# Performance work log

Hardware: AMD Instinct MI355X
Metric: run time of the kernel (lower is better)

## Reference

```python
import jax, jax.numpy as jnp
import numpy as np

D_MODEL = 1024
N_HEADS = 16
D_K = D_MODEL // N_HEADS


def setup_inputs() -> dict:
    key = jax.random.key(0)
    ks = jax.random.split(key, 12)
    B, S = 2, 2048
    scale = 1.0 / np.sqrt(D_MODEL)
    inp = {
        "q": jax.random.normal(ks[0], (B, S, D_MODEL), jnp.float32),
        "k": jax.random.normal(ks[1], (B, S, D_MODEL), jnp.float32),
        "v": jax.random.normal(ks[2], (B, S, D_MODEL), jnp.float32),
        "k_pe": jax.random.normal(ks[3], (N_HEADS, D_K, S), jnp.float32),
        "Wq": jax.random.normal(ks[4], (D_MODEL, D_MODEL), jnp.float32) * scale,
        "bq": jnp.zeros((D_MODEL,), jnp.float32),
        "Wk": jax.random.normal(ks[5], (D_MODEL, D_MODEL), jnp.float32) * scale,
        "bk": jnp.zeros((D_MODEL,), jnp.float32),
        "Wv": jax.random.normal(ks[6], (D_MODEL, D_MODEL), jnp.float32) * scale,
        "bv": jnp.zeros((D_MODEL,), jnp.float32),
        "Wo": jax.random.normal(ks[7], (D_MODEL, D_MODEL), jnp.float32) * scale,
        "bo": jnp.zeros((D_MODEL,), jnp.float32),
    }
    return inp


def reference(q, k, v, k_pe, Wq, bq, Wk, bk, Wv, bv, Wo, bo):
    B, S, _ = q.shape
    # projections -> [B, H, S, d_k]
    def split_heads(x):
        return x.reshape(B, S, N_HEADS, D_K).transpose(0, 2, 1, 3)
    qh = split_heads(q @ Wq + bq)
    kh = split_heads(k @ Wk + bk)
    vh = split_heads(v @ Wv + bv)
    # content scores + relative positional scores (two matmuls, summed)
    scores = jnp.einsum("bhsd,bhtd->bhst", qh, kh)
    scores = scores + jnp.einsum("bhsd,hdt->bhst", qh, k_pe)
    scores = scores / jnp.sqrt(jnp.asarray(D_K, qh.dtype))
    attn = jax.nn.softmax(scores, axis=-1)
    out = jnp.einsum("bhst,bhtd->bhsd", attn, vh)  # [B,H,S,d_k]
    out = out.transpose(0, 2, 1, 3).reshape(B, S, D_MODEL)
    return out @ Wo + bo
```

## Files before the change

### kernel.cpp

```cpp
#include <hip/hip_runtime.h>
#include <stdint.h>
#include <math.h>

typedef __bf16 bf16;
typedef __attribute__((ext_vector_type(8))) __bf16 bf16x8;
typedef __attribute__((ext_vector_type(4))) __bf16 bf16x4;
typedef __attribute__((ext_vector_type(4))) float f32x4;

#define MFMA_BF16(a, b, c) __builtin_amdgcn_mfma_f32_16x16x32_bf16((a), (b), (c), 0, 0, 0)

#if __has_builtin(__builtin_amdgcn_exp2f)
#define EXP2F __builtin_amdgcn_exp2f
#else
#define EXP2F exp2f
#endif

#define QSCALE 0.18033688011112042f

__device__ __forceinline__ void gl_lds16(const bf16* g, bf16* l) {
  __builtin_amdgcn_global_load_lds(
      (__attribute__((address_space(1))) unsigned int*)(uintptr_t)(g),
      (__attribute__((address_space(3))) unsigned int*)(l),
      16, 0, 0);
}

__global__ __launch_bounds__(256) void prep(
    const float* __restrict__ q, const float* __restrict__ k,
    const float* __restrict__ v, bf16* __restrict__ qb,
    bf16* __restrict__ kb, bf16* __restrict__ vb,
    const float* __restrict__ W0, const float* __restrict__ W1,
    const float* __restrict__ W2, const float* __restrict__ W3,
    bf16* __restrict__ Wt)
{
  __shared__ float tile[64][65];
  const int tid = threadIdx.x;
  const int bid = blockIdx.x;
  if (bid < 6144) {
    const int z = bid >> 11;
    const int idx = bid & 2047;
    const float* s = (z == 0) ? q : (z == 1) ? k : v;
    bf16* d = (z == 0) ? qb : (z == 1) ? kb : vb;
    size_t i = ((size_t)idx * 256 + tid) * 8;
    float4 a = *(const float4*)(s + i);
    float4 b = *(const float4*)(s + i + 4);
    bf16x8 o;
    o[0] = (bf16)a.x; o[1] = (bf16)a.y; o[2] = (bf16)a.z; o[3] = (bf16)a.w;
    o[4] = (bf16)b.x; o[5] = (bf16)b.y; o[6] = (bf16)b.z; o[7] = (bf16)b.w;
    *(bf16x8*)(d + i) = o;
  } else {
    const int t = bid - 6144;
    const int z = t >> 8;
    const int rem = t & 255;
    const int r0 = (rem >> 4) * 64, c0 = (rem & 15) * 64;
    const float* src = (z == 0) ? W0 : (z == 1) ? W1 : (z == 2) ? W2 : W3;
    bf16* dst = Wt + (size_t)z * (1024 * 1024);
#pragma unroll
    for (int h = 0; h < 2; ++h) {
      int qq = tid + h * 256;
      int row = qq >> 3, cc = qq & 7;
      float4 a = *(const float4*)(src + (size_t)(r0 + row) * 1024 + c0 + cc * 8);
      float4 b = *(const float4*)(src + (size_t)(r0 + row) * 1024 + c0 + cc * 8 + 4);
      tile[row][cc * 8 + 0] = a.x; tile[row][cc * 8 + 1] = a.y;
      tile[row][cc * 8 + 2] = a.z; tile[row][cc * 8 + 3] = a.w;
      tile[row][cc * 8 + 4] = b.x; tile[row][cc * 8 + 5] = b.y;
      tile[row][cc * 8 + 6] = b.z; tile[row][cc * 8 + 7] = b.w;
    }
    __syncthreads();
#pragma unroll
    for (int h = 0; h < 2; ++h) {
      int qq = tid + h * 256;
      int row = qq >> 3, cc = qq & 7;
      bf16x8 o;
#pragma unroll
      for (int e = 0; e < 8; ++e) o[e] = (bf16)tile[cc * 8 + e][row];
      *(bf16x8*)(dst + (size_t)(c0 + row) * 1024 + r0 + cc * 8) = o;
    }
  }
}

template <int MODE>
__device__ __forceinline__ void gemm_body(
    const bf16* __restrict__ A, const bf16* __restrict__ Wt,
    const float* __restrict__ bias, const float* __restrict__ kpe,
    void* __restrict__ out_v)
{
  __shared__ __align__(16) bf16 As[128 * 32];
  __shared__ __align__(16) bf16 Bs[128 * 32];
  const int tid = threadIdx.x;
  const int w = tid >> 6, lane = tid & 63;
  const int lm = lane & 15, quad = lane >> 4;
  const int wm = w >> 1, wn = w & 1;
  const int m0 = blockIdx.y * 128, n0 = blockIdx.x * 128;

  f32x4 zero4 = {0.f, 0.f, 0.f, 0.f};
  f32x4 acc[4][4];
#pragma unroll
  for (int i = 0; i < 4; ++i)
#pragma unroll
    for (int j = 0; j < 4; ++j) acc[i][j] = zero4;

  for (int kb = 0; kb < 32; ++kb) {
    __syncthreads();
#pragma unroll
    for (int h = 0; h < 2; ++h) {
      int qq = tid + h * 256;
      int row = qq >> 2, cs = qq & 3;
      int cc = cs ^ ((row >> 1) & 3);
      gl_lds16(A + (size_t)(m0 + row) * 1024 + kb * 32 + cc * 8, As + qq * 8);
      gl_lds16(Wt + (size_t)(n0 + row) * 1024 + kb * 32 + cc * 8, Bs + qq * 8);
    }
    __syncthreads();

    bf16x8 af[4], wf[4];
#pragma unroll
    for (int j = 0; j < 4; ++j) {
      int row = wm * 64 + j * 16 + lm;
      af[j] = *(const bf16x8*)(As + row * 32 + ((quad ^ ((row >> 1) & 3)) * 8));
    }
#pragma unroll
    for (int i = 0; i < 4; ++i) {
      int row = wn * 64 + i * 16 + lm;
      wf[i] = *(const bf16x8*)(Bs + row * 32 + ((quad ^ ((row >> 1) & 3)) * 8));
    }
#pragma unroll
    for (int i = 0; i < 4; ++i)
#pragma unroll
      for (int j = 0; j < 4; ++j) {
        if (MODE == 2)
          acc[i][j] = MFMA_BF16(af[j], wf[i], acc[i][j]);
        else
          acc[i][j] = MFMA_BF16(wf[i], af[j], acc[i][j]);
      }
  }

  if (MODE == 2) {
#pragma unroll
    for (int i = 0; i < 4; ++i) {
      const int ng = n0 + wn * 64 + i * 16 + lm;
      const int hh = ng >> 6, d = ng & 63;
      const float bv = bias[ng];
#pragma unroll
      for (int j = 0; j < 4; ++j) {
        const int mg = m0 + wm * 64 + j * 16 + quad * 4;
        const int b = mg >> 11, s = mg & 2047;
        bf16x4 o;
#pragma unroll
        for (int r = 0; r < 4; ++r) o[r] = (bf16)(acc[i][j][r] + bv);
        *(bf16x4*)((bf16*)out_v +
                   (((size_t)(b * 16 + hh)) * 64 + d) * 2048 + s) = o;
      }
    }
  } else {
#pragma unroll
    for (int i = 0; i < 4; ++i) {
      const int nb = n0 + wn * 64 + i * 16 + quad * 4;
      const float4 bv4 = *(const float4*)(bias + nb);
      const int hh = nb >> 6, db = nb & 63;
#pragma unroll
      for (int j = 0; j < 4; ++j) {
        const int mg = m0 + wm * 64 + j * 16 + lm;
        const int b = mg >> 11, s = mg & 2047;
        if (MODE == 3) {
          float4 o;
          o.x = acc[i][j][0] + bv4.x; o.y = acc[i][j][1] + bv4.y;
          o.z = acc[i][j][2] + bv4.z; o.w = acc[i][j][3] + bv4.w;
          *(float4*)((float*)out_v + (size_t)mg * 1024 + nb) = o;
        } else {
          bf16x4 o;
#pragma unroll
          for (int r = 0; r < 4; ++r) {
            float val = acc[i][j][r] + ((const float*)&bv4)[r];
            if (MODE == 0) val *= QSCALE;
            if (MODE == 1)
              val += kpe[((size_t)(hh * 64 + db + r)) * 2048 + s];
            o[r] = (bf16)val;
          }
          *(bf16x4*)((bf16*)out_v +
                     (((size_t)(b * 16 + hh)) * 2048 + s) * 64 + db) = o;
        }
      }
    }
  }
}

__global__ __launch_bounds__(256) void qkv_gemm(
    const bf16* __restrict__ qb, const bf16* __restrict__ kb, const bf16* __restrict__ vb,
    const bf16* __restrict__ Wt, const float* __restrict__ biq,
    const float* __restrict__ bik, const float* __restrict__ biv,
    const float* __restrict__ kpe,
    bf16* __restrict__ Qs, bf16* __restrict__ Ks, bf16* __restrict__ Vts)
{
  const int z = blockIdx.z;
  if (z == 0) {
    gemm_body<0>(qb, Wt, biq, nullptr, Qs);
  } else if (z == 1) {
    gemm_body<1>(kb, Wt + (size_t)1 * 1024 * 1024, bik, kpe, Ks);
  } else {
    gemm_body<2>(vb, Wt + (size_t)2 * 1024 * 1024, biv, nullptr, Vts);
  }
}

__global__ __launch_bounds__(256) void out_gemm(
    const bf16* __restrict__ A, const bf16* __restrict__ Wt,
    const float* __restrict__ bias, float* __restrict__ out)
{
  gemm_body<3>(A, Wt, bias, nullptr, out);
}

#define PST 76

__global__ __launch_bounds__(256) void flash_attn(
    const bf16* __restrict__ Q, const bf16* __restrict__ K,
    const bf16* __restrict__ Vt, bf16* __restrict__ O)
{
  __shared__ __align__(16) bf16 Qt[128 * 64];
  __shared__ __align__(16) bf16 Kt[64 * 64];
  __shared__ __align__(16) bf16 Vs[64 * 64];
  __shared__ __align__(16) bf16 Ps[128 * PST];

  const int tid = threadIdx.x;
  const int w = tid >> 6, lane = tid & 63;
  const int lm = lane & 15, quad = lane >> 4;
  const int bh = blockIdx.y;
  const int s0 = blockIdx.x * 128;
  const size_t qkbase = (size_t)bh * (2048 * 64);
  const size_t vbase = (size_t)bh * (64 * 2048);

#pragma unroll
  for (int h = 0; h < 4; ++h) {
    int qq = tid + h * 256;
    int row = qq >> 3, cs = qq & 7;
    int cc = cs ^ (row & 7);
    gl_lds16(Q + qkbase + (size_t)(s0 + row) * 64 + cc * 8, Qt + qq * 8);
  }
  __syncthreads();

  bf16x8 qa[2][2];
#pragma unroll
  for (int g = 0; g < 2; ++g) {
    int row = w * 32 + g * 16 + lm;
    qa[g][0] = *(const bf16x8*)(Qt + row * 64 + ((quad ^ (row & 7)) * 8));
    qa[g][1] = *(const bf16x8*)(Qt + row * 64 + (((quad + 4) ^ (row & 7)) * 8));
  }

  f32x4 zero4 = {0.f, 0.f, 0.f, 0.f};
  float l_part[2] = {0.f, 0.f};
  f32x4 oacc[2][4];
#pragma unroll
  for (int g = 0; g < 2; ++g)
#pragma unroll
    for (int dt = 0; dt < 4; ++dt) oacc[g][dt] = zero4;

  const int prow[2] = {(w * 32 + lm) * PST, (w * 32 + 16 + lm) * PST};

  for (int kt = 0; kt < 32; ++kt) {
    const int t0 = kt * 64;
    __syncthreads();
#pragma unroll
    for (int h = 0; h < 2; ++h) {
      int qq = tid + h * 256;
      int row = qq >> 3, cs = qq & 7;
      int cc = cs ^ (row & 7);
      gl_lds16(K + qkbase + (size_t)(t0 + row) * 64 + cc * 8, Kt + qq * 8);
      gl_lds16(Vt + vbase + (size_t)row * 2048 + t0 + cc * 8, Vs + qq * 8);
    }
    __syncthreads();

#pragma unroll
    for (int c = 0; c < 4; ++c) {
      int row = c * 16 + lm;
      bf16x8 kb0 = *(const bf16x8*)(Kt + row * 64 + ((quad ^ (row & 7)) * 8));
      bf16x8 kb1 = *(const bf16x8*)(Kt + row * 64 + (((quad + 4) ^ (row & 7)) * 8));
#pragma unroll
      for (int g = 0; g < 2; ++g) {
        f32x4 z = MFMA_BF16(kb0, qa[g][0], zero4);
        f32x4 st = MFMA_BF16(kb1, qa[g][1], z);
        bf16x4 pk;
#pragma unroll
        for (int r = 0; r < 4; ++r) {
          float p = EXP2F(st[r]);
          l_part[g] += p;
          pk[r] = (bf16)p;
        }
        *(bf16x4*)(Ps + prow[g] + c * 16 + quad * 4) = pk;
      }
    }

    bf16x8 pa[2][2];
#pragma unroll
    for (int g = 0; g < 2; ++g) {
      pa[g][0] = *(const bf16x8*)(Ps + prow[g] + quad * 8);
      pa[g][1] = *(const bf16x8*)(Ps + prow[g] + 32 + quad * 8);
    }
#pragma unroll
    for (int dt = 0; dt < 4; ++dt) {
      int row = dt * 16 + lm;
      bf16x8 va0 = *(const bf16x8*)(Vs + row * 64 + ((quad ^ (row & 7)) * 8));
      bf16x8 va1 = *(const bf16x8*)(Vs + row * 64 + (((quad + 4) ^ (row & 7)) * 8));
#pragma unroll
      for (int g = 0; g < 2; ++g) {
        oacc[g][dt] = MFMA_BF16(va0, pa[g][0], oacc[g][dt]);
        oacc[g][dt] = MFMA_BF16(va1, pa[g][1], oacc[g][dt]);
      }
    }
  }

  const int b = bh >> 4, hh = bh & 15;
#pragma unroll
  for (int g = 0; g < 2; ++g) {
    float l = l_part[g];
    l += __shfl_xor(l, 16, 64);
    l += __shfl_xor(l, 32, 64);
    float inv = 1.f / l;
#pragma unroll
    for (int dt = 0; dt < 4; ++dt)
#pragma unroll
      for (int r = 0; r < 4; ++r)
        Ps[prow[g] + dt * 16 + quad * 4 + r] = (bf16)(oacc[g][dt][r] * inv);

    const int srow = s0 + w * 32 + g * 16 + lm;
    const size_t ob = ((size_t)(b * 2048 + srow)) * 1024 + hh * 64;
#pragma unroll
    for (int half = 0; half < 2; ++half) {
      bf16x8 ov = *(const bf16x8*)(Ps + prow[g] + (half * 4 + quad) * 8);
      *(bf16x8*)(O + ob + (half * 4 + quad) * 8) = ov;
    }
  }
}

extern "C" void kernel_launch(void* const* d_in, const int* in_sizes, int n_in,
                              void* d_out, int out_size, void* d_ws, size_t ws_size,
                              hipStream_t stream) {
  (void)in_sizes; (void)n_in; (void)out_size; (void)ws_size;
  const float* q   = (const float*)d_in[0];
  const float* k   = (const float*)d_in[1];
  const float* v   = (const float*)d_in[2];
  const float* kpe = (const float*)d_in[3];
  const float* Wq  = (const float*)d_in[4];
  const float* bq  = (const float*)d_in[5];
  const float* Wk  = (const float*)d_in[6];
  const float* bk  = (const float*)d_in[7];
  const float* Wv  = (const float*)d_in[8];
  const float* bv  = (const float*)d_in[9];
  const float* Wo  = (const float*)d_in[10];
  const float* bo  = (const float*)d_in[11];

  const size_t NT = 4u * 1024 * 1024;
  bf16* ws  = (bf16*)d_ws;
  bf16* Wt  = ws;
  bf16* qb  = Wt + NT;
  bf16* kb  = qb + NT;
  bf16* vb  = kb + NT;
  bf16* Qs  = vb + NT;
  bf16* Ks  = Qs + NT;
  bf16* Vts = Ks + NT;
  bf16* Oa  = Vts + NT;

  prep<<<dim3(7168), 256, 0, stream>>>(q, k, v, qb, kb, vb, Wq, Wk, Wv, Wo, Wt);
  qkv_gemm<<<dim3(8, 32, 3), 256, 0, stream>>>(qb, kb, vb, Wt, bq, bk, bv, kpe,
                                               Qs, Ks, Vts);
  flash_attn<<<dim3(16, 32), 256, 0, stream>>>(Qs, Ks, Vts, Oa);
  out_gemm<<<dim3(8, 32), 256, 0, stream>>>(Oa, Wt + 3u * 1024 * 1024, bo,
                                            (float*)d_out);
}
```

Before: 250.3 us.

## Load attention K/V fragments directly to registers and retile output GEMM

Flash attention no longer stages Q, K and V through LDS with barriers each tile; each wave reads its MFMA fragments straight from global memory, with the loop unrolled by two so loads can overlap. The output projection gets its own kernel with a 128x64 tile and twice as many blocks, so more CUs are filled. The cost is redundant global/L2 traffic across waves, possibly uncoalesced fragment loads, and lower per-block reuse in the GEMM.

```diff
diff --git a/kernel.cpp b/kernel.cpp
--- a/kernel.cpp
+++ b/kernel.cpp
@@ -160,24 +160,17 @@
       for (int j = 0; j < 4; ++j) {
         const int mg = m0 + wm * 64 + j * 16 + lm;
         const int b = mg >> 11, s = mg & 2047;
-        if (MODE == 3) {
-          float4 o;
-          o.x = acc[i][j][0] + bv4.x; o.y = acc[i][j][1] + bv4.y;
-          o.z = acc[i][j][2] + bv4.z; o.w = acc[i][j][3] + bv4.w;
-          *(float4*)((float*)out_v + (size_t)mg * 1024 + nb) = o;
-        } else {
-          bf16x4 o;
-#pragma unroll
-          for (int r = 0; r < 4; ++r) {
-            float val = acc[i][j][r] + ((const float*)&bv4)[r];
-            if (MODE == 0) val *= QSCALE;
-            if (MODE == 1)
-              val += kpe[((size_t)(hh * 64 + db + r)) * 2048 + s];
-            o[r] = (bf16)val;
-          }
-          *(bf16x4*)((bf16*)out_v +
-                     (((size_t)(b * 16 + hh)) * 2048 + s) * 64 + db) = o;
+        bf16x4 o;
+#pragma unroll
+        for (int r = 0; r < 4; ++r) {
+          float val = acc[i][j][r] + ((const float*)&bv4)[r];
+          if (MODE == 0) val *= QSCALE;
+          if (MODE == 1)
+            val += kpe[((size_t)(hh * 64 + db + r)) * 2048 + s];
+          o[r] = (bf16)val;
         }
+        *(bf16x4*)((bf16*)out_v +
+                   (((size_t)(b * 16 + hh)) * 2048 + s) * 64 + db) = o;
       }
     }
   }
@@ -204,7 +197,67 @@
     const bf16* __restrict__ A, const bf16* __restrict__ Wt,
     const float* __restrict__ bias, float* __restrict__ out)
 {
-  gemm_body<3>(A, Wt, bias, nullptr, out);
+  __shared__ __align__(16) bf16 As[128 * 32];
+  __shared__ __align__(16) bf16 Bs[64 * 32];
+  const int tid = threadIdx.x;
+  const int w = tid >> 6, lane = tid & 63;
+  const int lm = lane & 15, quad = lane >> 4;
+  const int m0 = blockIdx.y * 128, n0 = blockIdx.x * 64;
+
+  f32x4 zero4 = {0.f, 0.f, 0.f, 0.f};
+  f32x4 acc[4][2];
+#pragma unroll
+  for (int i = 0; i < 4; ++i)
+#pragma unroll
+    for (int j = 0; j < 2; ++j) acc[i][j] = zero4;
+
+  for (int kb = 0; kb < 32; ++kb) {
+    __syncthreads();
+#pragma unroll
+    for (int h = 0; h < 2; ++h) {
+      int qq = tid + h * 256;
+      int row = qq >> 2, cs = qq & 3;
+      int cc = cs ^ ((row >> 1) & 3);
+      gl_lds16(A + (size_t)(m0 + row) * 1024 + kb * 32 + cc * 8, As + qq * 8);
+    }
+    {
+      int row = tid >> 2, cs = tid & 3;
+      int cc = cs ^ ((row >> 1) & 3);
+      gl_lds16(Wt + (size_t)(n0 + row) * 1024 + kb * 32 + cc * 8, Bs + tid * 8);
+    }
+    __syncthreads();
+
+    bf16x8 af[2], wf[4];
+#pragma unroll
+    for (int j = 0; j < 2; ++j) {
+      int row = w * 32 + j * 16 + lm;
+      af[j] = *(const bf16x8*)(As + row * 32 + ((quad ^ ((row >> 1) & 3)) * 8));
+    }
+#pragma unroll
+    for (int i = 0; i < 4; ++i) {
+      int row = i * 16 + lm;
+      wf[i] = *(const bf16x8*)(Bs + row * 32 + ((quad ^ ((row >> 1) & 3)) * 8));
+    }
+#pragma unroll
+    for (int i = 0; i < 4; ++i)
+#pragma unroll
+      for (int j = 0; j < 2; ++j)
+        acc[i][j] = MFMA_BF16(wf[i], af[j], acc[i][j]);
+  }
+
+#pragma unroll
+  for (int i = 0; i < 4; ++i) {
+    const int nb = n0 + i * 16 + quad * 4;
+    const float4 bv4 = *(const float4*)(bias + nb);
+#pragma unroll
+    for (int j = 0; j < 2; ++j) {
+      const int mg = m0 + w * 32 + j * 16 + lm;
+      float4 o;
+      o.x = acc[i][j][0] + bv4.x; o.y = acc[i][j][1] + bv4.y;
+      o.z = acc[i][j][2] + bv4.z; o.w = acc[i][j][3] + bv4.w;
+      *(float4*)(out + (size_t)mg * 1024 + nb) = o;
+    }
+  }
 }
 
 #define PST 76
@@ -213,9 +266,6 @@
     const bf16* __restrict__ Q, const bf16* __restrict__ K,
     const bf16* __restrict__ Vt, bf16* __restrict__ O)
 {
-  __shared__ __align__(16) bf16 Qt[128 * 64];
-  __shared__ __align__(16) bf16 Kt[64 * 64];
-  __shared__ __align__(16) bf16 Vs[64 * 64];
   __shared__ __align__(16) bf16 Ps[128 * PST];
 
   const int tid = threadIdx.x;
@@ -226,21 +276,12 @@
   const size_t qkbase = (size_t)bh * (2048 * 64);
   const size_t vbase = (size_t)bh * (64 * 2048);
 
-#pragma unroll
-  for (int h = 0; h < 4; ++h) {
-    int qq = tid + h * 256;
-    int row = qq >> 3, cs = qq & 7;
-    int cc = cs ^ (row & 7);
-    gl_lds16(Q + qkbase + (size_t)(s0 + row) * 64 + cc * 8, Qt + qq * 8);
-  }
-  __syncthreads();
-
   bf16x8 qa[2][2];
 #pragma unroll
   for (int g = 0; g < 2; ++g) {
-    int row = w * 32 + g * 16 + lm;
-    qa[g][0] = *(const bf16x8*)(Qt + row * 64 + ((quad ^ (row & 7)) * 8));
-    qa[g][1] = *(const bf16x8*)(Qt + row * 64 + (((quad + 4) ^ (row & 7)) * 8));
+    const bf16* qp = Q + qkbase + (size_t)(s0 + w * 32 + g * 16 + lm) * 64;
+    qa[g][0] = *(const bf16x8*)(qp + quad * 8);
+    qa[g][1] = *(const bf16x8*)(qp + 32 + quad * 8);
   }
 
   f32x4 zero4 = {0.f, 0.f, 0.f, 0.f};
@@ -253,28 +294,34 @@
 
   const int prow[2] = {(w * 32 + lm) * PST, (w * 32 + 16 + lm) * PST};
 
+  const bf16* kp = K + qkbase + (size_t)lm * 64 + quad * 8;
+  const bf16* vp = Vt + vbase + (size_t)lm * 2048 + quad * 8;
+
+#pragma unroll 2
   for (int kt = 0; kt < 32; ++kt) {
     const int t0 = kt * 64;
-    __syncthreads();
-#pragma unroll
-    for (int h = 0; h < 2; ++h) {
-      int qq = tid + h * 256;
-      int row = qq >> 3, cs = qq & 7;
-      int cc = cs ^ (row & 7);
-      gl_lds16(K + qkbase + (size_t)(t0 + row) * 64 + cc * 8, Kt + qq * 8);
-      gl_lds16(Vt + vbase + (size_t)row * 2048 + t0 + cc * 8, Vs + qq * 8);
-    }
-    __syncthreads();
-
+
+    bf16x8 kf[4][2];
 #pragma unroll
     for (int c = 0; c < 4; ++c) {
-      int row = c * 16 + lm;
-      bf16x8 kb0 = *(const bf16x8*)(Kt + row * 64 + ((quad ^ (row & 7)) * 8));
-      bf16x8 kb1 = *(const bf16x8*)(Kt + row * 64 + (((quad + 4) ^ (row & 7)) * 8));
+      const bf16* p = kp + (size_t)(t0 + c * 16) * 64;
+      kf[c][0] = *(const bf16x8*)(p);
+      kf[c][1] = *(const bf16x8*)(p + 32);
+    }
+    bf16x8 vf[4][2];
+#pragma unroll
+    for (int dt = 0; dt < 4; ++dt) {
+      const bf16* p = vp + (size_t)(dt * 16) * 2048 + t0;
+      vf[dt][0] = *(const bf16x8*)(p);
+      vf[dt][1] = *(const bf16x8*)(p + 32);
+    }
+
+#pragma unroll
+    for (int c = 0; c < 4; ++c) {
 #pragma unroll
       for (int g = 0; g < 2; ++g) {
-        f32x4 z = MFMA_BF16(kb0, qa[g][0], zero4);
-        f32x4 st = MFMA_BF16(kb1, qa[g][1], z);
+        f32x4 z = MFMA_BF16(kf[c][0], qa[g][0], zero4);
+        f32x4 st = MFMA_BF16(kf[c][1], qa[g][1], z);
         bf16x4 pk;
 #pragma unroll
         for (int r = 0; r < 4; ++r) {
@@ -293,16 +340,12 @@
       pa[g][1] = *(const bf16x8*)(Ps + prow[g] + 32 + quad * 8);
     }
 #pragma unroll
-    for (int dt = 0; dt < 4; ++dt) {
-      int row = dt * 16 + lm;
-      bf16x8 va0 = *(const bf16x8*)(Vs + row * 64 + ((quad ^ (row & 7)) * 8));
-      bf16x8 va1 = *(const bf16x8*)(Vs + row * 64 + (((quad + 4) ^ (row & 7)) * 8));
+    for (int dt = 0; dt < 4; ++dt)
 #pragma unroll
       for (int g = 0; g < 2; ++g) {
-        oacc[g][dt] = MFMA_BF16(va0, pa[g][0], oacc[g][dt]);
-        oacc[g][dt] = MFMA_BF16(va1, pa[g][1], oacc[g][dt]);
+        oacc[g][dt] = MFMA_BF16(vf[dt][0], pa[g][0], oacc[g][dt]);
+        oacc[g][dt] = MFMA_BF16(vf[dt][1], pa[g][1], oacc[g][dt]);
       }
-    }
   }
 
   const int b = bh >> 4, hh = bh & 15;
@@ -360,6 +403,6 @@
   qkv_gemm<<<dim3(8, 32, 3), 256, 0, stream>>>(qb, kb, vb, Wt, bq, bk, bv, kpe,
                                                Qs, Ks, Vts);
   flash_attn<<<dim3(16, 32), 256, 0, stream>>>(Qs, Ks, Vts, Oa);
-  out_gemm<<<dim3(8, 32), 256, 0, stream>>>(Oa, Wt + 3u * 1024 * 1024, bo,
-                                            (float*)d_out);
-}
+  out_gemm<<<dim3(16, 32), 256, 0, stream>>>(Oa, Wt + 3u * 1024 * 1024, bo,
+                                             (float*)d_out);
+}
```

Result: slower. 317.1 us (+26.7%).
